# Performance work log

Hardware: AMD Instinct MI355X
Metric: run time of the kernel (lower is better)

## Reference

```python
import jax, jax.numpy as jnp
import numpy as np

B = 2048   # jets (graphs)
P = 50     # particles per jet
N = B * P  # nodes
E = B * P * P  # within-jet all-pairs radius-graph edges (incl. self-loops)
H = 5      # edge-MLP width ([5,5,5,5] channel list)
EPS = 1e-5
NEG_SLOPE = 0.01


def _batchnorm(h, gamma, beta):
    # training-mode batch norm over the edge dimension (biased variance, as torch)
    mu = jnp.mean(h, axis=0)
    var = jnp.mean(h * h, axis=0) - mu * mu
    return gamma * (h - mu) * jax.lax.rsqrt(var + EPS) + beta


def setup_inputs() -> dict:
    key = jax.random.key(0)
    ks = jax.random.split(key, 16)
    # angles: per-jet center offset + tight spread so all within-jet pairs are inside dR=0.4
    centers = jax.random.normal(ks[0], (B, 1, 2), dtype=jnp.float32) + jnp.array([2.0, 0.5], dtype=jnp.float32)
    angles = (centers + 0.1 * jax.random.normal(ks[1], (B, P, 2), dtype=jnp.float32)).reshape(N, 2)
    pt = jax.random.uniform(ks[2], (N,), dtype=jnp.float32, minval=0.1, maxval=1.0)
    features = jnp.linalg.norm(angles, axis=-1, keepdims=True)  # rho = |view_as_complex(angles)|, [N,1]
    # radius graph: with the tight spread every within-jet pair is within dR -> fixed E
    ii = np.arange(P)
    pi, pj = np.meshgrid(ii, ii, indexing='ij')
    base = (np.arange(B, dtype=np.int64) * P)[:, None]
    src = (base + pj.ravel()[None, :]).ravel()  # x_j (source)
    dst = (base + pi.ravel()[None, :]).ravel()  # x_i (target) = aggregation index
    edge_index = jnp.asarray(np.stack([src, dst]), dtype=jnp.int32)  # [2, E]
    def lin(k, o, i):
        return (jax.random.normal(k, (o, i), dtype=jnp.float32) / np.sqrt(i)).astype(jnp.float32)
    W1 = lin(ks[3], H, 5); b1 = jnp.zeros((H,), jnp.float32)
    W2 = lin(ks[4], H, H); b2 = jnp.zeros((H,), jnp.float32)
    W3 = lin(ks[5], H, H); b3 = jnp.zeros((H,), jnp.float32)
    g1 = jnp.ones((H,), jnp.float32); bt1 = jnp.zeros((H,), jnp.float32)
    g2 = jnp.ones((H,), jnp.float32); bt2 = jnp.zeros((H,), jnp.float32)
    return {"pt": pt, "features": features, "angles": angles,
            "W1": W1, "b1": b1, "g1": g1, "bt1": bt1,
            "W2": W2, "b2": b2, "g2": g2, "bt2": bt2,
            "W3": W3, "b3": b3, "edge_index": edge_index}


def reference(pt, features, angles, W1, b1, g1, bt1, W2, b2, g2, bt2, W3, b3, edge_index):
    src = edge_index[0]  # j (source)
    dst = edge_index[1]  # i (target, aggregation index)
    x = jnp.concatenate([pt[:, None], features, angles], axis=1)  # [N, 4]
    xi = x[dst]  # [E, 4]
    xj = x[src]
    # complex ratio angles_i / angles_j in real arithmetic
    ar, ai = xi[:, 2], xi[:, 3]
    br, bi = xj[:, 2], xj[:, 3]
    den = br * br + bi * bi
    dr = (ar * br + ai * bi) / den
    di = (ai * br - ar * bi) / den
    fi = xi[:, 1:2]
    fj = xj[:, 1:2]
    mlp_in = jnp.concatenate([fi, fj, fj - fi, dr[:, None], di[:, None]], axis=1)  # [E, 5]
    h = jax.nn.leaky_relu(_batchnorm(mlp_in @ W1.T + b1, g1, bt1), NEG_SLOPE)
    h = jax.nn.leaky_relu(_batchnorm(h @ W2.T + b2, g2, bt2), NEG_SLOPE)
    h = h @ W3.T + b3  # [E, 5]
    msg = jnp.concatenate([xi[:, :1], h, xi[:, 2:4]], axis=1)  # [E, 8]
    pt_e = msg[:, 0]
    denom = jax.ops.segment_sum(pt_e, dst, num_segments=N)  # [N]
    wj = pt_e / denom[dst]
    agg = jax.ops.segment_sum(wj[:, None] * msg, dst, num_segments=N)  # [N, 8]
    # exp(2*pi*i*theta) * z with theta = agg[:, -3], z = complex(agg[:, -2:])
    theta = agg[:, 5]
    zr, zi = agg[:, 6], agg[:, 7]
    c = jnp.cos(2.0 * jnp.pi * theta)
    s = jnp.sin(2.0 * jnp.pi * theta)
    out = jnp.concatenate([agg[:, :5], (c * zr - s * zi)[:, None], (c * zi + s * zr)[:, None]], axis=1)  # [N, 7]
    return out
```

## Files before the change

kernel.cpp:

```cpp
#include <hip/hip_runtime.h>

#define PP 50
#define TPB 256
#define NBATCH 2048
#define GB 2
#define NBLK2 (NBATCH / GB)
#define NBLK1 512
#define NCOPY 64

static constexpr float EPSF = 1e-5f;
static constexpr double INV_ETOT = 1.0 / 5120000.0;

static __device__ __forceinline__ float lrelu(float x) {
    return fmaxf(x, 0.0f) + 0.01f * fminf(x, 0.0f);
}
static __device__ __forceinline__ float rfl(float x) {
    return __int_as_float(__builtin_amdgcn_readfirstlane(__float_as_int(x)));
}


__global__ __launch_bounds__(TPB) void stats1_kernel(
    const float* __restrict__ feat, const float* __restrict__ ang,
    const float* __restrict__ W1, const float* __restrict__ b1,
    double* __restrict__ acc)
{
    __shared__ double bacc[4][10];
    const int t = threadIdx.x;
    const int lane = t & 63;
    const int wv = t >> 6;

    float v0[5], v1[5], v2[5], v3[5], bb1[5];
#pragma unroll
    for (int o = 0; o < 5; ++o) {
        v0[o] = rfl(W1[o*5+0] - W1[o*5+2]);
        v1[o] = rfl(W1[o*5+1] + W1[o*5+2]);
        v2[o] = rfl(W1[o*5+3]);
        v3[o] = rfl(W1[o*5+4]);
        bb1[o] = rfl(b1[o]);
    }

    float f = 0.f, zr = 0.f, zi = 0.f, inv = 0.f;
    if (lane < PP) {
        const int idx = (blockIdx.x * 4 + wv) * PP + lane;
        f = feat[idx];
        float2 a2 = ((const float2*)ang)[idx];
        zr = a2.x; zi = a2.y;
        inv = 1.0f / (zr*zr + zi*zi);
    }
    const float wr = zr * inv, wi = -zi * inv;

    float p[16] = { f, f*f, zr, zi, wr, wi, f*zr, f*zi, f*wr, f*wi,
                    zr*zr, zi*zi, zr*zi, wr*wr, wi*wi, wr*wi };
#pragma unroll
    for (int k = 0; k < 16; ++k) {
        float v = p[k];
#pragma unroll
        for (int off = 32; off > 0; off >>= 1) v += __shfl_down(v, off, 64);
        p[k] = v;
    }
    if (lane == 0) {
        const double P0 = p[0], P1 = p[1], P2 = p[2], P3 = p[3], P4 = p[4];
        const double P5 = p[5], P6 = p[6], P7 = p[7], P8 = p[8], P9 = p[9];
        const double P10 = p[10], P11 = p[11], P12 = p[12];
        const double P13 = p[13], P14 = p[14], P15 = p[15];
        const double Sfi = 50.0 * P0;
        const double Sdr = P2*P4 - P3*P5;
        const double Sdi = P3*P4 + P2*P5;
        const double m00 = 50.0 * P1, m11 = m00, m01 = P0*P0;
        const double m02 = P6*P4 - P7*P5;
        const double m03 = P7*P4 + P6*P5;
        const double m12 = P2*P8 - P3*P9;
        const double m13 = P3*P8 + P2*P9;
        const double m22 = P10*P13 - 2.0*P12*P15 + P11*P14;
        const double m33 = P11*P13 + 2.0*P12*P15 + P10*P14;
        const double m23 = P12*P13 + P10*P15 - P11*P15 - P12*P14;
#pragma unroll
        for (int o = 0; o < 5; ++o) {
            const double a0=v0[o], a1=v1[o], a2=v2[o], a3=v3[o], bo=bb1[o];
            const double sy = a0*Sfi + a1*Sfi + a2*Sdr + a3*Sdi + 2500.0*bo;
            const double q  = a0*a0*m00 + a1*a1*m11 + a2*a2*m22 + a3*a3*m33
                           + 2.0*(a0*a1*m01 + a0*a2*m02 + a0*a3*m03
                                + a1*a2*m12 + a1*a3*m13 + a2*a3*m23);
            bacc[wv][o]   = sy;
            bacc[wv][5+o] = q + 2.0*bo*sy - 2500.0*bo*bo;
        }
    }
    __syncthreads();
    if (t < 10) {
        double s = bacc[0][t] + bacc[1][t] + bacc[2][t] + bacc[3][t];
        atomicAdd(&acc[t * NCOPY + (blockIdx.x & (NCOPY-1))], s);
    }
}

__global__ __launch_bounds__(TPB, 2) void pass2_kernel(
    const float* __restrict__ feat, const float* __restrict__ ang,
    const float* __restrict__ W1, const float* __restrict__ b1,
    const float* __restrict__ g1, const float* __restrict__ bt1,
    const float* __restrict__ W2, const float* __restrict__ b2,
    double* __restrict__ acc)
{
    __shared__ float4 nd[GB * PP];
    __shared__ double tmp[10];
    __shared__ float red[4][10];
    const int t = threadIdx.x;

    if (t < GB * PP) {
        const int idx = blockIdx.x * (GB * PP) + t;
        float f = feat[idx];
        float2 a2 = ((const float2*)ang)[idx];
        nd[t] = make_float4(f, a2.x, a2.y, 1.0f / (a2.x*a2.x + a2.y*a2.y));
    } else if (t >= 128 && t < 138) {
        const int k = t - 128;
        double s = 0.0;
#pragma unroll
        for (int c = 0; c < NCOPY; ++c) s += acc[k * NCOPY + c];
        tmp[k] = s;
    }

    float v0[5], v1[5], v2[5], v3[5], bb1[5], w2[25], bb2[5];
#pragma unroll
    for (int o = 0; o < 5; ++o) {
        v0[o] = rfl(W1[o*5+0] - W1[o*5+2]);
        v1[o] = rfl(W1[o*5+1] + W1[o*5+2]);
        v2[o] = rfl(W1[o*5+3]);
        v3[o] = rfl(W1[o*5+4]);
        bb1[o] = rfl(b1[o]); bb2[o] = rfl(b2[o]);
    }
#pragma unroll
    for (int i = 0; i < 25; ++i) w2[i] = rfl(W2[i]);

    __syncthreads();

    float sc1[5], sh1[5];
#pragma unroll
    for (int o = 0; o < 5; ++o) {
        double mu  = tmp[o]   * INV_ETOT;
        double var = tmp[5+o] * INV_ETOT - mu * mu;
        float sc = rfl(g1[o]) * rsqrtf((float)var + EPSF);
        sc1[o] = rfl(sc);
        sh1[o] = rfl(rfl(bt1[o]) - (float)mu * sc);
    }

    float a[10];
#pragma unroll
    for (int k = 0; k < 10; ++k) a[k] = 0.f;

    if (t < 250) {
        const int pi = t / 5;
        const int s5 = t - pi*5;
#pragma unroll
        for (int g = 0; g < GB; ++g) {
            const float4 ni = nd[g*PP + pi];
            const float fi = ni.x, ari = ni.y, aii = ni.z;
            float4 njs[10];
#pragma unroll
            for (int q = 0; q < 10; ++q) njs[q] = nd[g*PP + s5*10 + q];
#pragma unroll
            for (int q = 0; q < 10; ++q) {
                const float4 nj = njs[q];
                const float dr = fmaf(ari, nj.y,  aii*nj.z) * nj.w;
                const float di = fmaf(aii, nj.y, -ari*nj.z) * nj.w;
                float h1[5];
#pragma unroll
                for (int o = 0; o < 5; ++o) {
                    float y = fmaf(v0[o], fi, fmaf(v1[o], nj.x,
                              fmaf(v2[o], dr, fmaf(v3[o], di, bb1[o]))));
                    h1[o] = lrelu(fmaf(y, sc1[o], sh1[o]));
                }
#pragma unroll
                for (int o = 0; o < 5; ++o) {
                    float y = bb2[o];
                    y = fmaf(w2[o*5+0], h1[0], y);
                    y = fmaf(w2[o*5+1], h1[1], y);
                    y = fmaf(w2[o*5+2], h1[2], y);
                    y = fmaf(w2[o*5+3], h1[3], y);
                    y = fmaf(w2[o*5+4], h1[4], y);
                    a[o]   += y;
                    a[5+o]  = fmaf(y, y, a[5+o]);
                }
            }
        }
    }

#pragma unroll
    for (int k = 0; k < 10; ++k) {
        float v = a[k];
#pragma unroll
        for (int off = 32; off > 0; off >>= 1) v += __shfl_down(v, off, 64);
        a[k] = v;
    }
    const int lane = t & 63, wv = t >> 6;
    if (lane == 0) {
#pragma unroll
        for (int k = 0; k < 10; ++k) red[wv][k] = a[k];
    }
    __syncthreads();
    if (t < 10) {
        atomicAdd(&acc[(10 + t) * NCOPY + (blockIdx.x & (NCOPY-1))],
                  (double)(red[0][t] + red[1][t] + red[2][t] + red[3][t]));
    }
}

__global__ __launch_bounds__(TPB, 2) void pass3_kernel(
    const float* __restrict__ pt,
    const float* __restrict__ feat, const float* __restrict__ ang,
    const float* __restrict__ W1, const float* __restrict__ b1,
    const float* __restrict__ g1, const float* __restrict__ bt1,
    const float* __restrict__ W2, const float* __restrict__ b2,
    const float* __restrict__ g2, const float* __restrict__ bt2,
    const float* __restrict__ W3, const float* __restrict__ b3,
    const double* __restrict__ acc, float* __restrict__ out)
{
    __shared__ float4 nd[GB * PP];
    __shared__ float spt[GB * PP];
    __shared__ double tmp[20];
    __shared__ float part[250][5];
    const int t = threadIdx.x;

    if (t < GB * PP) {
        const int idx = blockIdx.x * (GB * PP) + t;
        float f = feat[idx];
        float2 a2 = ((const float2*)ang)[idx];
        nd[t] = make_float4(f, a2.x, a2.y, 1.0f / (a2.x*a2.x + a2.y*a2.y));
        spt[t] = pt[idx];
    } else if (t >= 128 && t < 148) {
        const int k = t - 128;
        double s = 0.0;
#pragma unroll
        for (int c = 0; c < NCOPY; ++c) s += acc[k * NCOPY + c];
        tmp[k] = s;
    }

    float v0[5], v1[5], v2[5], v3[5], bb1[5], w2[25], bb2[5], w3[25], bb3[5];
#pragma unroll
    for (int o = 0; o < 5; ++o) {
        v0[o] = rfl(W1[o*5+0] - W1[o*5+2]);
        v1[o] = rfl(W1[o*5+1] + W1[o*5+2]);
        v2[o] = rfl(W1[o*5+3]);
        v3[o] = rfl(W1[o*5+4]);
        bb1[o] = rfl(b1[o]); bb2[o] = rfl(b2[o]); bb3[o] = rfl(b3[o]);
    }
#pragma unroll
    for (int i = 0; i < 25; ++i) { w2[i] = rfl(W2[i]); w3[i] = rfl(W3[i]); }

    __syncthreads();

    float sc1[5], sh1[5], sc2[5], sh2[5];
#pragma unroll
    for (int o = 0; o < 5; ++o) {
        double mu1  = tmp[o]    * INV_ETOT;
        double var1 = tmp[5+o]  * INV_ETOT - mu1 * mu1;
        float s1 = rfl(g1[o]) * rsqrtf((float)var1 + EPSF);
        sc1[o] = rfl(s1);
        sh1[o] = rfl(rfl(bt1[o]) - (float)mu1 * s1);
        double mu2  = tmp[10+o] * INV_ETOT;
        double var2 = tmp[15+o] * INV_ETOT - mu2 * mu2;
        float s2 = rfl(g2[o]) * rsqrtf((float)var2 + EPSF);
        sc2[o] = rfl(s2);
        sh2[o] = rfl(rfl(bt2[o]) - (float)mu2 * s2);
    }

    const int pi = t / 5;
    const int s5 = t - pi*5;

#pragma unroll
    for (int g = 0; g < GB; ++g) {
        float a[5] = {0.f, 0.f, 0.f, 0.f, 0.f};
        if (t < 250) {
            const float4 ni = nd[g*PP + pi];
            const float fi = ni.x, ari = ni.y, aii = ni.z;
            float4 njs[10];
#pragma unroll
            for (int q = 0; q < 10; ++q) njs[q] = nd[g*PP + s5*10 + q];
#pragma unroll
            for (int q = 0; q < 10; ++q) {
                const float4 nj = njs[q];
                const float dr = fmaf(ari, nj.y,  aii*nj.z) * nj.w;
                const float di = fmaf(aii, nj.y, -ari*nj.z) * nj.w;
                float h1[5], h2[5];
#pragma unroll
                for (int o = 0; o < 5; ++o) {
                    float y = fmaf(v0[o], fi, fmaf(v1[o], nj.x,
                              fmaf(v2[o], dr, fmaf(v3[o], di, bb1[o]))));
                    h1[o] = lrelu(fmaf(y, sc1[o], sh1[o]));
                }
#pragma unroll
                for (int o = 0; o < 5; ++o) {
                    float y = bb2[o];
                    y = fmaf(w2[o*5+0], h1[0], y);
                    y = fmaf(w2[o*5+1], h1[1], y);
                    y = fmaf(w2[o*5+2], h1[2], y);
                    y = fmaf(w2[o*5+3], h1[3], y);
                    y = fmaf(w2[o*5+4], h1[4], y);
                    h2[o] = lrelu(fmaf(y, sc2[o], sh2[o]));
                }
#pragma unroll
                for (int o = 0; o < 5; ++o) {
                    float y = bb3[o];
                    y = fmaf(w3[o*5+0], h2[0], y);
                    y = fmaf(w3[o*5+1], h2[1], y);
                    y = fmaf(w3[o*5+2], h2[2], y);
                    y = fmaf(w3[o*5+3], h2[3], y);
                    y = fmaf(w3[o*5+4], h2[4], y);
                    a[o] += y;
                }
            }
#pragma unroll
            for (int c = 0; c < 5; ++c) part[t][c] = a[c];
        }
        __syncthreads();

        if (t < PP) {
            float m[5];
#pragma unroll
            for (int c = 0; c < 5; ++c) {
                m[c] = (part[5*t][c] + part[5*t+1][c] + part[5*t+2][c] +
                        part[5*t+3][c] + part[5*t+4][c]) * 0.02f;
            }
            const int node = g*PP + t;
            const int d = blockIdx.x * (GB * PP) + node;
            const float4 ni = nd[node];
            float ss, cc;
            sincosf(6.2831853071795865f * m[4], &ss, &cc);
            float* o = out + (size_t)d * 7;
            o[0] = spt[node];
            o[1] = m[0];
            o[2] = m[1];
            o[3] = m[2];
            o[4] = m[3];
            o[5] = cc * ni.y - ss * ni.z;
            o[6] = cc * ni.z + ss * ni.y;
        }
        __syncthreads();
    }
}

extern "C" void kernel_launch(void* const* d_in, const int* in_sizes, int n_in,
                              void* d_out, int out_size, void* d_ws, size_t ws_size,
                              hipStream_t stream)
{
    const float* pt   = (const float*)d_in[0];
    const float* feat = (const float*)d_in[1];
    const float* ang  = (const float*)d_in[2];
    const float* W1   = (const float*)d_in[3];
    const float* b1   = (const float*)d_in[4];
    const float* g1   = (const float*)d_in[5];
    const float* bt1  = (const float*)d_in[6];
    const float* W2   = (const float*)d_in[7];
    const float* b2   = (const float*)d_in[8];
    const float* g2   = (const float*)d_in[9];
    const float* bt2  = (const float*)d_in[10];
    const float* W3   = (const float*)d_in[11];
    const float* b3   = (const float*)d_in[12];
    float* out = (float*)d_out;
    double* acc = (double*)d_ws;

    hipMemsetAsync(d_ws, 0, 20 * NCOPY * sizeof(double), stream);
    stats1_kernel<<<NBLK1, TPB, 0, stream>>>(feat, ang, W1, b1, acc);
    pass2_kernel<<<NBLK2, TPB, 0, stream>>>(feat, ang, W1, b1, g1, bt1, W2, b2, acc);
    pass3_kernel<<<NBLK2, TPB, 0, stream>>>(pt, feat, ang, W1, b1, g1, bt1, W2, b2,
                                            g2, bt2, W3, b3, acc, out);
}
```

Before: 143.8 us.

## Fold batchnorm into weights, use second-moment stats, hoist final linear layer

Pass2 now gathers the first and second moments of the layer-1 activations (sum and the 15-entry upper-triangle Gram), and pass3 derives the layer-2 batchnorm statistics from them. This drops the per-edge W2 matvec from pass2. Both batchnorms are folded into the weights and biases, and the final W3 linear layer moves after the mean aggregation so it runs once per node instead of once per edge. Leaky ReLU is reduced to a single max, and the 1/|a_j|^2 factor is pre-multiplied into the source angles. The cost is more shuffle reductions and atomics (20 instead of 10) in pass2, plus some precision risk from computing the variance as q - mu^2.

```diff
diff --git a/kernel.cpp b/kernel.cpp
--- a/kernel.cpp
+++ b/kernel.cpp
@@ -7,12 +7,13 @@
 #define NBLK2 (NBATCH / GB)
 #define NBLK1 512
 #define NCOPY 64
+#define NSLOT 30
 
 static constexpr float EPSF = 1e-5f;
 static constexpr double INV_ETOT = 1.0 / 5120000.0;
 
 static __device__ __forceinline__ float lrelu(float x) {
-    return fmaxf(x, 0.0f) + 0.01f * fminf(x, 0.0f);
+    return fmaxf(x, 0.01f * x);
 }
 static __device__ __forceinline__ float rfl(float x) {
     return __int_as_float(__builtin_amdgcn_readfirstlane(__float_as_int(x)));
@@ -96,19 +97,21 @@
     const float* __restrict__ feat, const float* __restrict__ ang,
     const float* __restrict__ W1, const float* __restrict__ b1,
     const float* __restrict__ g1, const float* __restrict__ bt1,
-    const float* __restrict__ W2, const float* __restrict__ b2,
     double* __restrict__ acc)
 {
     __shared__ float4 nd[GB * PP];
+    __shared__ float4 ndj[GB * PP];
     __shared__ double tmp[10];
-    __shared__ float red[4][10];
+    __shared__ float red[4][20];
     const int t = threadIdx.x;
 
     if (t < GB * PP) {
         const int idx = blockIdx.x * (GB * PP) + t;
         float f = feat[idx];
         float2 a2 = ((const float2*)ang)[idx];
-        nd[t] = make_float4(f, a2.x, a2.y, 1.0f / (a2.x*a2.x + a2.y*a2.y));
+        float inv = 1.0f / (a2.x*a2.x + a2.y*a2.y);
+        nd[t]  = make_float4(f, a2.x, a2.y, 0.0f);
+        ndj[t] = make_float4(f, a2.x * inv, a2.y * inv, 0.0f);
     } else if (t >= 128 && t < 138) {
         const int k = t - 128;
         double s = 0.0;
@@ -117,33 +120,35 @@
         tmp[k] = s;
     }
 
-    float v0[5], v1[5], v2[5], v3[5], bb1[5], w2[25], bb2[5];
+    float v0[5], v1[5], v2[5], v3[5], bb1[5];
 #pragma unroll
     for (int o = 0; o < 5; ++o) {
         v0[o] = rfl(W1[o*5+0] - W1[o*5+2]);
         v1[o] = rfl(W1[o*5+1] + W1[o*5+2]);
         v2[o] = rfl(W1[o*5+3]);
         v3[o] = rfl(W1[o*5+4]);
-        bb1[o] = rfl(b1[o]); bb2[o] = rfl(b2[o]);
-    }
-#pragma unroll
-    for (int i = 0; i < 25; ++i) w2[i] = rfl(W2[i]);
+        bb1[o] = rfl(b1[o]);
+    }
 
     __syncthreads();
 
-    float sc1[5], sh1[5];
 #pragma unroll
     for (int o = 0; o < 5; ++o) {
         double mu  = tmp[o]   * INV_ETOT;
         double var = tmp[5+o] * INV_ETOT - mu * mu;
         float sc = rfl(g1[o]) * rsqrtf((float)var + EPSF);
-        sc1[o] = rfl(sc);
-        sh1[o] = rfl(rfl(bt1[o]) - (float)mu * sc);
-    }
-
-    float a[10];
-#pragma unroll
-    for (int k = 0; k < 10; ++k) a[k] = 0.f;
+        float sh = rfl(rfl(bt1[o]) - (float)mu * sc);
+        v0[o] = rfl(v0[o] * sc);
+        v1[o] = rfl(v1[o] * sc);
+        v2[o] = rfl(v2[o] * sc);
+        v3[o] = rfl(v3[o] * sc);
+        bb1[o] = rfl(fmaf(bb1[o], sc, sh));
+    }
+
+    float s1[5] = {0.f, 0.f, 0.f, 0.f, 0.f};
+    float mm[15];
+#pragma unroll
+    for (int k = 0; k < 15; ++k) mm[k] = 0.f;
 
     if (t < 250) {
         const int pi = t / 5;
@@ -154,36 +159,39 @@
             const float fi = ni.x, ari = ni.y, aii = ni.z;
             float4 njs[10];
 #pragma unroll
-            for (int q = 0; q < 10; ++q) njs[q] = nd[g*PP + s5*10 + q];
+            for (int q = 0; q < 10; ++q) njs[q] = ndj[g*PP + s5*10 + q];
 #pragma unroll
             for (int q = 0; q < 10; ++q) {
                 const float4 nj = njs[q];
-                const float dr = fmaf(ari, nj.y,  aii*nj.z) * nj.w;
-                const float di = fmaf(aii, nj.y, -ari*nj.z) * nj.w;
+                const float dr = fmaf(ari, nj.y,  aii*nj.z);
+                const float di = fmaf(aii, nj.y, -ari*nj.z);
                 float h1[5];
 #pragma unroll
                 for (int o = 0; o < 5; ++o) {
                     float y = fmaf(v0[o], fi, fmaf(v1[o], nj.x,
                               fmaf(v2[o], dr, fmaf(v3[o], di, bb1[o]))));
-                    h1[o] = lrelu(fmaf(y, sc1[o], sh1[o]));
+                    h1[o] = lrelu(y);
                 }
 #pragma unroll
-                for (int o = 0; o < 5; ++o) {
-                    float y = bb2[o];
-                    y = fmaf(w2[o*5+0], h1[0], y);
-                    y = fmaf(w2[o*5+1], h1[1], y);
-                    y = fmaf(w2[o*5+2], h1[2], y);
-                    y = fmaf(w2[o*5+3], h1[3], y);
-                    y = fmaf(w2[o*5+4], h1[4], y);
-                    a[o]   += y;
-                    a[5+o]  = fmaf(y, y, a[5+o]);
+                for (int k = 0; k < 5; ++k) {
+                    s1[k] += h1[k];
+#pragma unroll
+                    for (int l = k; l < 5; ++l) {
+                        const int idx = k*5 - (k*(k+1))/2 + l;
+                        mm[idx] = fmaf(h1[k], h1[l], mm[idx]);
+                    }
                 }
             }
         }
     }
 
-#pragma unroll
-    for (int k = 0; k < 10; ++k) {
+    float a[20];
+#pragma unroll
+    for (int k = 0; k < 5; ++k) a[k] = s1[k];
+#pragma unroll
+    for (int k = 0; k < 15; ++k) a[5+k] = mm[k];
+#pragma unroll
+    for (int k = 0; k < 20; ++k) {
         float v = a[k];
 #pragma unroll
         for (int off = 32; off > 0; off >>= 1) v += __shfl_down(v, off, 64);
@@ -192,10 +200,10 @@
     const int lane = t & 63, wv = t >> 6;
     if (lane == 0) {
 #pragma unroll
-        for (int k = 0; k < 10; ++k) red[wv][k] = a[k];
+        for (int k = 0; k < 20; ++k) red[wv][k] = a[k];
     }
     __syncthreads();
-    if (t < 10) {
+    if (t < 20) {
         atomicAdd(&acc[(10 + t) * NCOPY + (blockIdx.x & (NCOPY-1))],
                   (double)(red[0][t] + red[1][t] + red[2][t] + red[3][t]));
     }
@@ -212,8 +220,10 @@
     const double* __restrict__ acc, float* __restrict__ out)
 {
     __shared__ float4 nd[GB * PP];
+    __shared__ float4 ndj[GB * PP];
     __shared__ float spt[GB * PP];
-    __shared__ double tmp[20];
+    __shared__ double tmp[NSLOT];
+    __shared__ float scsh[4][5];
     __shared__ float part[250][5];
     const int t = threadIdx.x;
 
@@ -221,9 +231,11 @@
         const int idx = blockIdx.x * (GB * PP) + t;
         float f = feat[idx];
         float2 a2 = ((const float2*)ang)[idx];
-        nd[t] = make_float4(f, a2.x, a2.y, 1.0f / (a2.x*a2.x + a2.y*a2.y));
+        float inv = 1.0f / (a2.x*a2.x + a2.y*a2.y);
+        nd[t]  = make_float4(f, a2.x, a2.y, 0.0f);
+        ndj[t] = make_float4(f, a2.x * inv, a2.y * inv, 0.0f);
         spt[t] = pt[idx];
-    } else if (t >= 128 && t < 148) {
+    } else if (t >= 128 && t < 128 + NSLOT) {
         const int k = t - 128;
         double s = 0.0;
 #pragma unroll
@@ -245,19 +257,55 @@
 
     __syncthreads();
 
-    float sc1[5], sh1[5], sc2[5], sh2[5];
+    if (t < 5) {
+        const int o = t;
+        double mu1  = tmp[o]   * INV_ETOT;
+        double var1 = tmp[5+o] * INV_ETOT - mu1 * mu1;
+        float sc1 = g1[o] * rsqrtf((float)var1 + EPSF);
+        scsh[0][o] = sc1;
+        scsh[1][o] = bt1[o] - (float)mu1 * sc1;
+
+        double w[5], Sn[5];
+#pragma unroll
+        for (int k = 0; k < 5; ++k) {
+            w[k]  = (double)w2[o*5+k];
+            Sn[k] = tmp[10+k] * INV_ETOT;
+        }
+        double muw = 0.0;
+#pragma unroll
+        for (int k = 0; k < 5; ++k) muw += w[k] * Sn[k];
+        double q = 0.0;
+#pragma unroll
+        for (int k = 0; k < 5; ++k) {
+#pragma unroll
+            for (int l = k; l < 5; ++l) {
+                const int idx = k*5 - (k*(k+1))/2 + l;
+                const double Mn = tmp[15+idx] * INV_ETOT;
+                q += (k == l ? w[k]*w[k] : 2.0*w[k]*w[l]) * Mn;
+            }
+        }
+        double var2 = q - muw * muw;
+        double mu2  = muw + (double)bb2[o];
+        float sc2 = g2[o] * rsqrtf((float)var2 + EPSF);
+        scsh[2][o] = sc2;
+        scsh[3][o] = bt2[o] - (float)mu2 * sc2;
+    }
+    __syncthreads();
+
 #pragma unroll
     for (int o = 0; o < 5; ++o) {
-        double mu1  = tmp[o]    * INV_ETOT;
-        double var1 = tmp[5+o]  * INV_ETOT - mu1 * mu1;
-        float s1 = rfl(g1[o]) * rsqrtf((float)var1 + EPSF);
-        sc1[o] = rfl(s1);
-        sh1[o] = rfl(rfl(bt1[o]) - (float)mu1 * s1);
-        double mu2  = tmp[10+o] * INV_ETOT;
-        double var2 = tmp[15+o] * INV_ETOT - mu2 * mu2;
-        float s2 = rfl(g2[o]) * rsqrtf((float)var2 + EPSF);
-        sc2[o] = rfl(s2);
-        sh2[o] = rfl(rfl(bt2[o]) - (float)mu2 * s2);
+        const float s1f = rfl(scsh[0][o]);
+        const float s1h = rfl(scsh[1][o]);
+        v0[o] = rfl(v0[o] * s1f);
+        v1[o] = rfl(v1[o] * s1f);
+        v2[o] = rfl(v2[o] * s1f);
+        v3[o] = rfl(v3[o] * s1f);
+        bb1[o] = rfl(fmaf(bb1[o], s1f, s1h));
+        const float s2f = rfl(scsh[2][o]);
+        const float s2h = rfl(scsh[3][o]);
+#pragma unroll
+        for (int k = 0; k < 5; ++k) w2[o*5+k] = rfl(w2[o*5+k] * s2f);
+        bb2[o] = rfl(fmaf(bb2[o], s2f, s2h));
     }
 
     const int pi = t / 5;
@@ -271,18 +319,18 @@
             const float fi = ni.x, ari = ni.y, aii = ni.z;
             float4 njs[10];
 #pragma unroll
-            for (int q = 0; q < 10; ++q) njs[q] = nd[g*PP + s5*10 + q];
+            for (int q = 0; q < 10; ++q) njs[q] = ndj[g*PP + s5*10 + q];
 #pragma unroll
             for (int q = 0; q < 10; ++q) {
                 const float4 nj = njs[q];
-                const float dr = fmaf(ari, nj.y,  aii*nj.z) * nj.w;
-                const float di = fmaf(aii, nj.y, -ari*nj.z) * nj.w;
+                const float dr = fmaf(ari, nj.y,  aii*nj.z);
+                const float di = fmaf(aii, nj.y, -ari*nj.z);
                 float h1[5], h2[5];
 #pragma unroll
                 for (int o = 0; o < 5; ++o) {
                     float y = fmaf(v0[o], fi, fmaf(v1[o], nj.x,
                               fmaf(v2[o], dr, fmaf(v3[o], di, bb1[o]))));
-                    h1[o] = lrelu(fmaf(y, sc1[o], sh1[o]));
+                    h1[o] = lrelu(y);
                 }
 #pragma unroll
                 for (int o = 0; o < 5; ++o) {
@@ -292,18 +340,10 @@
                     y = fmaf(w2[o*5+2], h1[2], y);
                     y = fmaf(w2[o*5+3], h1[3], y);
                     y = fmaf(w2[o*5+4], h1[4], y);
-                    h2[o] = lrelu(fmaf(y, sc2[o], sh2[o]));
+                    h2[o] = lrelu(y);
                 }
 #pragma unroll
-                for (int o = 0; o < 5; ++o) {
-                    float y = bb3[o];
-                    y = fmaf(w3[o*5+0], h2[0], y);
-                    y = fmaf(w3[o*5+1], h2[1], y);
-                    y = fmaf(w3[o*5+2], h2[2], y);
-                    y = fmaf(w3[o*5+3], h2[3], y);
-                    y = fmaf(w3[o*5+4], h2[4], y);
-                    a[o] += y;
-                }
+                for (int o = 0; o < 5; ++o) a[o] += h2[o];
             }
 #pragma unroll
             for (int c = 0; c < 5; ++c) part[t][c] = a[c];
@@ -311,11 +351,22 @@
         __syncthreads();
 
         if (t < PP) {
+            float hm[5];
+#pragma unroll
+            for (int c = 0; c < 5; ++c) {
+                hm[c] = (part[5*t][c] + part[5*t+1][c] + part[5*t+2][c] +
+                         part[5*t+3][c] + part[5*t+4][c]) * 0.02f;
+            }
             float m[5];
 #pragma unroll
             for (int c = 0; c < 5; ++c) {
-                m[c] = (part[5*t][c] + part[5*t+1][c] + part[5*t+2][c] +
-                        part[5*t+3][c] + part[5*t+4][c]) * 0.02f;
+                float y = bb3[c];
+                y = fmaf(w3[c*5+0], hm[0], y);
+                y = fmaf(w3[c*5+1], hm[1], y);
+                y = fmaf(w3[c*5+2], hm[2], y);
+                y = fmaf(w3[c*5+3], hm[3], y);
+                y = fmaf(w3[c*5+4], hm[4], y);
+                m[c] = y;
             }
             const int node = g*PP + t;
             const int d = blockIdx.x * (GB * PP) + node;
@@ -355,9 +406,9 @@
     float* out = (float*)d_out;
     double* acc = (double*)d_ws;
 
-    hipMemsetAsync(d_ws, 0, 20 * NCOPY * sizeof(double), stream);
+    hipMemsetAsync(d_ws, 0, NSLOT * NCOPY * sizeof(double), stream);
     stats1_kernel<<<NBLK1, TPB, 0, stream>>>(feat, ang, W1, b1, acc);
-    pass2_kernel<<<NBLK2, TPB, 0, stream>>>(feat, ang, W1, b1, g1, bt1, W2, b2, acc);
+    pass2_kernel<<<NBLK2, TPB, 0, stream>>>(feat, ang, W1, b1, g1, bt1, acc);
     pass3_kernel<<<NBLK2, TPB, 0, stream>>>(pt, feat, ang, W1, b1, g1, bt1, W2, b2,
                                             g2, bt2, W3, b3, acc, out);
 }
```

Result: faster. 140.5 us (-2.3%).
